# Optimization experiments

Hardware: AMD Instinct MI355X
Metric: run time of the kernel (lower is better)

## Reference

```python
import jax, jax.numpy as jnp
import numpy as np


def setup_inputs() -> dict:
    key = jax.random.key(0)
    k1, k2, k3, k4 = jax.random.split(key, 4)
    B, D, N, M = 4, 256, 4096, 4096
    return {
        "src": jax.random.normal(k1, (B, 3, N), dtype=jnp.float32),
        "tgt": jax.random.normal(k2, (B, 3, M), dtype=jnp.float32),
        "src_emb": jax.random.normal(k3, (B, D, N), dtype=jnp.float32),
        "tgt_emb": jax.random.normal(k4, (B, D, M), dtype=jnp.float32),
    }


def reference(src, tgt, src_emb, tgt_emb):
    # pairwise_distance[b,n,m] = -||src_emb[:,n] - tgt_emb[:,m]||^2
    # decomposed as -xx + 2*inner - yy (inner below is -2*dot, as in torch code)
    inner = -2.0 * jnp.einsum("bdn,bdm->bnm", src_emb, tgt_emb)       # [B,N,M]
    xx = jnp.sum(src_emb ** 2, axis=1)[:, :, None]                     # [B,N,1]
    yy = jnp.sum(tgt_emb ** 2, axis=1)[:, None, :]                     # [B,1,M]
    pairwise_distance = -xx - inner - yy                               # [B,N,M]
    scores = jax.nn.softmax(pairwise_distance, axis=2)                 # softmax over tgt points
    # src_corr[b,c,n] = sum_m tgt[b,c,m] * scores[b,n,m]
    src_corr = jnp.einsum("bcm,bnm->bcn", tgt, scores)                 # [B,3,N]
    return src_corr
```

## Files before the change

### kernel.cpp

```cpp
#include <hip/hip_runtime.h>

#define NBATCH 4
#define DDIM   256
#define NN     4096
#define MM     4096
#define NCHUNK 8
#define MCHUNK 512
#define MTILE  32
#define LOG2E  1.44269504088896340736f

using half8   = __attribute__((ext_vector_type(8))) _Float16;
using floatx4 = __attribute__((ext_vector_type(4))) float;


__global__ __launch_bounds__(256) void k_prep(const float* __restrict__ src_emb,
                                              const float* __restrict__ tgt_emb,
                                              const float* __restrict__ tgt,
                                              _Float16* __restrict__ Qf,
                                              _Float16* __restrict__ Kf,
                                              float* __restrict__ yyS,
                                              float4* __restrict__ Vt) {
    __shared__ __align__(16) float tile[128 * 64];
    __shared__ float psum[4][64];
    int i = blockIdx.x;
    int tensor = i & 1, b = (i >> 1) & 3, dg = (i >> 3) & 1, ng = i >> 4;
    int t = threadIdx.x, w = t >> 6, lane = t & 63;
    const float* in = tensor ? tgt_emb : src_emb;
    _Float16* outp  = tensor ? Kf : Qf;
    const float scale = tensor ? 1.0f : 2.0f * LOG2E;

    const char* gb = (const char*)(in + ((size_t)b * DDIM + dg * 128 + w * 32) * NN + ng * 64);
    char* lb = (char*)tile + w * 8192;
#pragma unroll
    for (int it = 0; it < 8; it++) {
        __builtin_amdgcn_global_load_lds(
            (const __attribute__((address_space(1))) uint32_t*)(const void*)
                (gb + (size_t)(it * 4 + (lane >> 4)) * (NN * 4) + (lane & 15) * 16),
            (__attribute__((address_space(3))) uint32_t*)(void*)
                (lb + it * 1024),
            16, 0, 0);
    }
    __syncthreads();

    float ss = 0.f;
    half8* ob = (half8*)(outp + (size_t)b * NN * DDIM);
    int n_glob = ng * 64 + lane;
    int blk = n_glob >> 4, l15 = n_glob & 15;
#pragma unroll
    for (int q = 0; q < 4; q++) {
        int octg = w * 4 + q;
        half8 v;
#pragma unroll
        for (int k = 0; k < 8; k++) {
            float f = tile[(octg * 8 + k) * 64 + lane];
            ss = fmaf(f, f, ss);
            v[k] = (_Float16)(f * scale);
        }
        int dglob = dg * 128 + octg * 8;
        int dsg = dglob >> 5, oct = (dglob >> 3) & 3;
        ob[(((size_t)blk * 8 + dsg) * 4 + oct) * 16 + l15] = v;
    }
    if (tensor) {
        psum[w][lane] = ss;
        __syncthreads();
        if (t < 64) {
            float s = psum[0][t] + psum[1][t] + psum[2][t] + psum[3][t];
            s *= -LOG2E;
            int m = ng * 64 + t;
            if (dg == 0) {
                const float* tp = tgt + (size_t)b * 3 * MM + m;
                Vt[(size_t)b * MM + m] = make_float4(tp[0], tp[MM], tp[2 * MM], s);
            } else {
                yyS[(size_t)b * MM + m] = s;
            }
        }
    }
}

__global__ __launch_bounds__(256, 4) void k_flash(const _Float16* __restrict__ Qf,
                                                  const _Float16* __restrict__ Kf,
                                                  const float* __restrict__ yyS,
                                                  const float4* __restrict__ Vt,
                                                  float4* __restrict__ Opart,
                                                  float* __restrict__ Mpart) {
    __shared__ __align__(16) _Float16 Kt[2][MTILE * DDIM];
    __shared__ floatx4 vtt[MCHUNK];

    int i = blockIdx.x, t = threadIdx.x;
    int xcd = i & 7, j = i >> 3;
    int b = xcd >> 1, nhalf = xcd & 1;
    int chunk = j & 7, ntile = nhalf * 16 + (j >> 3);

    int wave = t >> 6, lane = t & 63, quad = lane >> 4, l15 = lane & 15;
    int m0 = chunk * MCHUNK;
    int mblk0 = m0 >> 4;

    const char* kfb = (const char*)(Kf + (size_t)b * NN * DDIM);
    auto stage = [&](int mt) {
        const char* gb = kfb + (size_t)(mblk0 + mt * 2) * 8192 + wave * 4096;
        char* lb = (char*)&Kt[mt & 1][0] + wave * 4096;
#pragma unroll
        for (int it = 0; it < 4; it++) {
            __builtin_amdgcn_global_load_lds(
                (const __attribute__((address_space(1))) uint32_t*)(const void*)
                    (gb + it * 1024 + lane * 16),
                (__attribute__((address_space(3))) uint32_t*)(void*)
                    (lb + it * 1024),
                16, 0, 0);
        }
    };

    stage(0);

    {
        const float4* vb = Vt + (size_t)b * MM + m0;
        const float* yb = yyS + (size_t)b * MM + m0;
        for (int r = t; r < MCHUNK; r += 256) {
            float4 g = vb[r];
            vtt[r] = (floatx4){g.x, g.y, g.z, g.w + yb[r]};
        }
    }

    int nblk0 = ntile * 8 + wave * 2;
    const half8* qp = (const half8*)Qf + (size_t)b * NN * 32;
    half8 qf[2][8];
#pragma unroll
    for (int nb = 0; nb < 2; nb++)
#pragma unroll
        for (int ds = 0; ds < 8; ds++)
            qf[nb][ds] = qp[(((size_t)(nblk0 + nb) * 8 + ds) * 4 + quad) * 16 + l15];
#pragma unroll
    for (int nb = 0; nb < 2; nb++)
#pragma unroll
        for (int ds = 0; ds < 8; ds++)
            asm volatile("" : "+v"(qf[nb][ds]));

    const floatx4 z4 = {0.f, 0.f, 0.f, 0.f};
    floatx4 o[2] = {z4, z4};
    float mr[2] = {-__builtin_inff(), -__builtin_inff()};

    for (int mt = 0; mt < MCHUNK / MTILE; mt++) {
        __syncthreads();
        if (mt + 1 < MCHUNK / MTILE) stage(mt + 1);

        const char* Kb = (const char*)&Kt[mt & 1][0];
        floatx4 acc[2][2] = {{z4, z4}, {z4, z4}};
#pragma unroll
        for (int mb = 0; mb < 2; mb++) {
            const char* rb = Kb + mb * 8192 + lane * 16;
#pragma unroll
            for (int ds = 0; ds < 8; ds++) {
                half8 a = *(const half8*)(rb + ds * 1024);
                acc[mb][0] = __builtin_amdgcn_mfma_f32_16x16x32_f16(a, qf[0][ds], acc[mb][0], 0, 0, 0);
                acc[mb][1] = __builtin_amdgcn_mfma_f32_16x16x32_f16(a, qf[1][ds], acc[mb][1], 0, 0, 0);
            }
        }

        int vbase = mt * MTILE;
        float yv[8];
#pragma unroll
        for (int r = 0; r < 4; r++) {
            yv[r]     = ((const float*)&vtt[vbase + quad * 4 + r])[3];
            yv[4 + r] = ((const float*)&vtt[vbase + 16 + quad * 4 + r])[3];
        }
#pragma unroll
        for (int nb = 0; nb < 2; nb++) {
#pragma unroll
            for (int r = 0; r < 4; r++) {
                acc[0][nb][r] += yv[r];
                acc[1][nb][r] += yv[4 + r];
            }
            float tm = fmaxf(fmaxf(fmaxf(acc[0][nb][0], acc[0][nb][1]),
                                   fmaxf(acc[0][nb][2], acc[0][nb][3])),
                             fmaxf(fmaxf(acc[1][nb][0], acc[1][nb][1]),
                                   fmaxf(acc[1][nb][2], acc[1][nb][3])));
            float mn = fmaxf(mr[nb], tm);
            float al = __builtin_amdgcn_exp2f(mr[nb] - mn);
            mr[nb] = mn;
            o[nb] = o[nb] * al;
        }
#pragma unroll
        for (int jj = 0; jj < 8; jj++) {
            floatx4 vr = vtt[vbase + (jj >> 2) * 16 + quad * 4 + (jj & 3)];
#pragma unroll
            for (int nb = 0; nb < 2; nb++) {
                float p = __builtin_amdgcn_exp2f(acc[jj >> 2][nb][jj & 3] - mr[nb]);
                o[nb][0] = fmaf(p, vr[0], o[nb][0]);
                o[nb][1] = fmaf(p, vr[1], o[nb][1]);
                o[nb][2] = fmaf(p, vr[2], o[nb][2]);
                o[nb][3] += p;
            }
        }
    }

#pragma unroll
    for (int nb = 0; nb < 2; nb++) {
        float mq = mr[nb];
        float ma = fmaxf(mq, __shfl_xor(mq, 16, 64));
        ma = fmaxf(ma, __shfl_xor(ma, 32, 64));
        float wgt = __builtin_amdgcn_exp2f(mq - ma);
        floatx4 ow = o[nb] * wgt;
#pragma unroll
        for (int c = 0; c < 4; c++) {
            float v = ow[c];
            v += __shfl_xor(v, 16, 64);
            v += __shfl_xor(v, 32, 64);
            ow[c] = v;
        }
        if (quad == 0) {
            int n = (nblk0 + nb) * 16 + l15;
            size_t idx = (size_t)(chunk * NBATCH + b) * NN + n;
            Opart[idx] = make_float4(ow[0], ow[1], ow[2], ow[3]);
            Mpart[idx] = ma;
        }
    }
}

__global__ __launch_bounds__(128) void k_combine(const float4* __restrict__ Opart,
                                                 const float* __restrict__ Mpart,
                                                 float* __restrict__ out) {
    int idx = blockIdx.x * 128 + threadIdx.x;
    int b = idx >> 12, n = idx & (NN - 1);
    float mstar = -__builtin_inff();
#pragma unroll
    for (int j = 0; j < NCHUNK; j++)
        mstar = fmaxf(mstar, Mpart[(size_t)(j * NBATCH + b) * NN + n]);
    float o0 = 0.f, o1 = 0.f, o2 = 0.f, l = 0.f;
#pragma unroll
    for (int j = 0; j < NCHUNK; j++) {
        size_t id = (size_t)(j * NBATCH + b) * NN + n;
        float w = __builtin_amdgcn_exp2f(Mpart[id] - mstar);
        float4 P = Opart[id];
        o0 = fmaf(w, P.x, o0); o1 = fmaf(w, P.y, o1);
        o2 = fmaf(w, P.z, o2); l  = fmaf(w, P.w, l);
    }
    out[(size_t)(b * 3 + 0) * NN + n] = o0 / l;
    out[(size_t)(b * 3 + 1) * NN + n] = o1 / l;
    out[(size_t)(b * 3 + 2) * NN + n] = o2 / l;
}

extern "C" void kernel_launch(void* const* d_in, const int* in_sizes, int n_in,
                              void* d_out, int out_size, void* d_ws, size_t ws_size,
                              hipStream_t stream) {
    const float* tgt     = (const float*)d_in[1];
    const float* src_emb = (const float*)d_in[2];
    const float* tgt_emb = (const float*)d_in[3];
    float* out = (float*)d_out;

    char* ws = (char*)d_ws;
    _Float16* Qf  = (_Float16*)(ws);
    _Float16* Kf  = (_Float16*)(ws + 8388608);
    float*    yyS = (float*)   (ws + 16777216);
    float4*   Vt  = (float4*)  (ws + 16842752);
    float4*   Op  = (float4*)  (ws + 17104896);
    float*    Mp  = (float*)   (ws + 19202048);

    hipLaunchKernelGGL(k_prep,    dim3(1024), dim3(256), 0, stream,
                       src_emb, tgt_emb, tgt, Qf, Kf, yyS, Vt);
    hipLaunchKernelGGL(k_flash,   dim3(1024), dim3(256), 0, stream, Qf, Kf, yyS, Vt, Op, Mp);
    hipLaunchKernelGGL(k_combine, dim3(128),  dim3(128), 0, stream, Op, Mp, out);
}
```

Baseline: 133.9 us.

## Fuse Q fp16 conversion into flash kernel, drop Qf workspace pass

The prep kernel no longer converts src_emb to a blocked fp16 Qf buffer. Instead each flash block loads its query fragment straight from fp32 src_emb, scales it and converts it in registers. This removes a full write and read of the Q buffer and halves the prep grid. The cost is strided, uncoalesced fp32 loads in the flash prologue, repeated across the 8 m-chunks that share each query tile. The change also raises wave priority around the MFMA loop with s_setprio and replaces the launch-bounds occupancy hint with amdgpu_waves_per_eu(4,4).

New measurement: 152.5 us. 1.14x slower.

```diff
diff --git a/kernel.cpp b/kernel.cpp
--- a/kernel.cpp
+++ b/kernel.cpp
@@ -13,23 +13,18 @@
 using floatx4 = __attribute__((ext_vector_type(4))) float;
 
 
-__global__ __launch_bounds__(256) void k_prep(const float* __restrict__ src_emb,
-                                              const float* __restrict__ tgt_emb,
+__global__ __launch_bounds__(256) void k_prep(const float* __restrict__ tgt_emb,
                                               const float* __restrict__ tgt,
-                                              _Float16* __restrict__ Qf,
                                               _Float16* __restrict__ Kf,
                                               float* __restrict__ yyS,
                                               float4* __restrict__ Vt) {
     __shared__ __align__(16) float tile[128 * 64];
     __shared__ float psum[4][64];
     int i = blockIdx.x;
-    int tensor = i & 1, b = (i >> 1) & 3, dg = (i >> 3) & 1, ng = i >> 4;
+    int b = i & 3, dg = (i >> 2) & 1, ng = i >> 3;
     int t = threadIdx.x, w = t >> 6, lane = t & 63;
-    const float* in = tensor ? tgt_emb : src_emb;
-    _Float16* outp  = tensor ? Kf : Qf;
-    const float scale = tensor ? 1.0f : 2.0f * LOG2E;
-
-    const char* gb = (const char*)(in + ((size_t)b * DDIM + dg * 128 + w * 32) * NN + ng * 64);
+
+    const char* gb = (const char*)(tgt_emb + ((size_t)b * DDIM + dg * 128 + w * 32) * NN + ng * 64);
     char* lb = (char*)tile + w * 8192;
 #pragma unroll
     for (int it = 0; it < 8; it++) {
@@ -43,7 +38,7 @@
     __syncthreads();
 
     float ss = 0.f;
-    half8* ob = (half8*)(outp + (size_t)b * NN * DDIM);
+    half8* ob = (half8*)(Kf + (size_t)b * NN * DDIM);
     int n_glob = ng * 64 + lane;
     int blk = n_glob >> 4, l15 = n_glob & 15;
 #pragma unroll
@@ -54,35 +49,34 @@
         for (int k = 0; k < 8; k++) {
             float f = tile[(octg * 8 + k) * 64 + lane];
             ss = fmaf(f, f, ss);
-            v[k] = (_Float16)(f * scale);
+            v[k] = (_Float16)f;
         }
         int dglob = dg * 128 + octg * 8;
         int dsg = dglob >> 5, oct = (dglob >> 3) & 3;
         ob[(((size_t)blk * 8 + dsg) * 4 + oct) * 16 + l15] = v;
     }
-    if (tensor) {
-        psum[w][lane] = ss;
-        __syncthreads();
-        if (t < 64) {
-            float s = psum[0][t] + psum[1][t] + psum[2][t] + psum[3][t];
-            s *= -LOG2E;
-            int m = ng * 64 + t;
-            if (dg == 0) {
-                const float* tp = tgt + (size_t)b * 3 * MM + m;
-                Vt[(size_t)b * MM + m] = make_float4(tp[0], tp[MM], tp[2 * MM], s);
-            } else {
-                yyS[(size_t)b * MM + m] = s;
-            }
-        }
-    }
-}
-
-__global__ __launch_bounds__(256, 4) void k_flash(const _Float16* __restrict__ Qf,
-                                                  const _Float16* __restrict__ Kf,
-                                                  const float* __restrict__ yyS,
-                                                  const float4* __restrict__ Vt,
-                                                  float4* __restrict__ Opart,
-                                                  float* __restrict__ Mpart) {
+    psum[w][lane] = ss;
+    __syncthreads();
+    if (t < 64) {
+        float s = (psum[0][t] + psum[1][t]) + (psum[2][t] + psum[3][t]);
+        s *= -LOG2E;
+        int m = ng * 64 + t;
+        if (dg == 0) {
+            const float* tp = tgt + (size_t)b * 3 * MM + m;
+            Vt[(size_t)b * MM + m] = make_float4(tp[0], tp[MM], tp[2 * MM], s);
+        } else {
+            yyS[(size_t)b * MM + m] = s;
+        }
+    }
+}
+
+__global__ __launch_bounds__(256) __attribute__((amdgpu_waves_per_eu(4, 4)))
+void k_flash(const float* __restrict__ src_emb,
+             const _Float16* __restrict__ Kf,
+             const float* __restrict__ yyS,
+             const float4* __restrict__ Vt,
+             float4* __restrict__ Opart,
+             float* __restrict__ Mpart) {
     __shared__ __align__(16) _Float16 Kt[2][MTILE * DDIM];
     __shared__ floatx4 vtt[MCHUNK];
 
@@ -122,13 +116,21 @@
     }
 
     int nblk0 = ntile * 8 + wave * 2;
-    const half8* qp = (const half8*)Qf + (size_t)b * NN * 32;
+    const float* qsrc = src_emb + (size_t)b * DDIM * NN;
     half8 qf[2][8];
 #pragma unroll
-    for (int nb = 0; nb < 2; nb++)
-#pragma unroll
-        for (int ds = 0; ds < 8; ds++)
-            qf[nb][ds] = qp[(((size_t)(nblk0 + nb) * 8 + ds) * 4 + quad) * 16 + l15];
+    for (int nb = 0; nb < 2; nb++) {
+        int n = (nblk0 + nb) * 16 + l15;
+#pragma unroll
+        for (int ds = 0; ds < 8; ds++) {
+            const float* qp = qsrc + (size_t)(ds * 32 + quad * 8) * NN + n;
+            half8 v;
+#pragma unroll
+            for (int k = 0; k < 8; k++)
+                v[k] = (_Float16)(qp[(size_t)k * NN] * (2.0f * LOG2E));
+            qf[nb][ds] = v;
+        }
+    }
 #pragma unroll
     for (int nb = 0; nb < 2; nb++)
 #pragma unroll
@@ -145,6 +147,7 @@
 
         const char* Kb = (const char*)&Kt[mt & 1][0];
         floatx4 acc[2][2] = {{z4, z4}, {z4, z4}};
+        __builtin_amdgcn_s_setprio(1);
 #pragma unroll
         for (int mb = 0; mb < 2; mb++) {
             const char* rb = Kb + mb * 8192 + lane * 16;
@@ -155,6 +158,7 @@
                 acc[mb][1] = __builtin_amdgcn_mfma_f32_16x16x32_f16(a, qf[1][ds], acc[mb][1], 0, 0, 0);
             }
         }
+        __builtin_amdgcn_s_setprio(0);
 
         int vbase = mt * MTILE;
         float yv[8];
@@ -248,15 +252,15 @@
     float* out = (float*)d_out;
 
     char* ws = (char*)d_ws;
-    _Float16* Qf  = (_Float16*)(ws);
-    _Float16* Kf  = (_Float16*)(ws + 8388608);
-    float*    yyS = (float*)   (ws + 16777216);
-    float4*   Vt  = (float4*)  (ws + 16842752);
-    float4*   Op  = (float4*)  (ws + 17104896);
-    float*    Mp  = (float*)   (ws + 19202048);
-
-    hipLaunchKernelGGL(k_prep,    dim3(1024), dim3(256), 0, stream,
-                       src_emb, tgt_emb, tgt, Qf, Kf, yyS, Vt);
-    hipLaunchKernelGGL(k_flash,   dim3(1024), dim3(256), 0, stream, Qf, Kf, yyS, Vt, Op, Mp);
+    _Float16* Kf  = (_Float16*)(ws);
+    float*    yyS = (float*)   (ws + 8388608);
+    float4*   Vt  = (float4*)  (ws + 8454144);
+    float4*   Op  = (float4*)  (ws + 8716288);
+    float*    Mp  = (float*)   (ws + 10813440);
+
+    hipLaunchKernelGGL(k_prep,    dim3(512),  dim3(256), 0, stream,
+                       tgt_emb, tgt, Kf, yyS, Vt);
+    hipLaunchKernelGGL(k_flash,   dim3(1024), dim3(256), 0, stream,
+                       src_emb, Kf, yyS, Vt, Op, Mp);
     hipLaunchKernelGGL(k_combine, dim3(128),  dim3(128), 0, stream, Op, Mp, out);
 }
```

## Halve per-wave query rows in flash kernel and double grid size

Applied to the files above, without the earlier changes.

Each wave now handles one 16-row query block instead of two, so the flash kernel launches twice as many workgroups and each holds half the Q fragments and accumulators in registers. This cuts register pressure and raises parallelism, but every K tile staged into shared memory is reused by half as many MFMAs, so K traffic per output row doubles. It also raises wave priority around the MFMA loop with s_setprio and reassociates a small sum in the prep kernel.

Result: no change. 134.8 us (+0.6%).

```diff
diff --git a/kernel.cpp b/kernel.cpp
--- a/kernel.cpp
+++ b/kernel.cpp
@@ -64,7 +64,7 @@
         psum[w][lane] = ss;
         __syncthreads();
         if (t < 64) {
-            float s = psum[0][t] + psum[1][t] + psum[2][t] + psum[3][t];
+            float s = (psum[0][t] + psum[1][t]) + (psum[2][t] + psum[3][t]);
             s *= -LOG2E;
             int m = ng * 64 + t;
             if (dg == 0) {
@@ -89,7 +89,7 @@
     int i = blockIdx.x, t = threadIdx.x;
     int xcd = i & 7, j = i >> 3;
     int b = xcd >> 1, nhalf = xcd & 1;
-    int chunk = j & 7, ntile = nhalf * 16 + (j >> 3);
+    int chunk = j & 7, ntile = nhalf * 32 + (j >> 3);
 
     int wave = t >> 6, lane = t & 63, quad = lane >> 4, l15 = lane & 15;
     int m0 = chunk * MCHUNK;
@@ -121,40 +121,34 @@
         }
     }
 
-    int nblk0 = ntile * 8 + wave * 2;
+    int nblk = ntile * 4 + wave;
     const half8* qp = (const half8*)Qf + (size_t)b * NN * 32;
-    half8 qf[2][8];
-#pragma unroll
-    for (int nb = 0; nb < 2; nb++)
-#pragma unroll
-        for (int ds = 0; ds < 8; ds++)
-            qf[nb][ds] = qp[(((size_t)(nblk0 + nb) * 8 + ds) * 4 + quad) * 16 + l15];
-#pragma unroll
-    for (int nb = 0; nb < 2; nb++)
-#pragma unroll
-        for (int ds = 0; ds < 8; ds++)
-            asm volatile("" : "+v"(qf[nb][ds]));
+    half8 qf[8];
+#pragma unroll
+    for (int ds = 0; ds < 8; ds++)
+        qf[ds] = qp[(((size_t)nblk * 8 + ds) * 4 + quad) * 16 + l15];
 
     const floatx4 z4 = {0.f, 0.f, 0.f, 0.f};
-    floatx4 o[2] = {z4, z4};
-    float mr[2] = {-__builtin_inff(), -__builtin_inff()};
+    floatx4 o = z4;
+    float mr = -__builtin_inff();
 
     for (int mt = 0; mt < MCHUNK / MTILE; mt++) {
         __syncthreads();
         if (mt + 1 < MCHUNK / MTILE) stage(mt + 1);
 
         const char* Kb = (const char*)&Kt[mt & 1][0];
-        floatx4 acc[2][2] = {{z4, z4}, {z4, z4}};
+        floatx4 acc[2] = {z4, z4};
+        __builtin_amdgcn_s_setprio(1);
 #pragma unroll
         for (int mb = 0; mb < 2; mb++) {
             const char* rb = Kb + mb * 8192 + lane * 16;
 #pragma unroll
             for (int ds = 0; ds < 8; ds++) {
                 half8 a = *(const half8*)(rb + ds * 1024);
-                acc[mb][0] = __builtin_amdgcn_mfma_f32_16x16x32_f16(a, qf[0][ds], acc[mb][0], 0, 0, 0);
-                acc[mb][1] = __builtin_amdgcn_mfma_f32_16x16x32_f16(a, qf[1][ds], acc[mb][1], 0, 0, 0);
+                acc[mb] = __builtin_amdgcn_mfma_f32_16x16x32_f16(a, qf[ds], acc[mb], 0, 0, 0);
             }
         }
+        __builtin_amdgcn_s_setprio(0);
 
         int vbase = mt * MTILE;
         float yv[8];
@@ -164,42 +158,33 @@
             yv[4 + r] = ((const float*)&vtt[vbase + 16 + quad * 4 + r])[3];
         }
 #pragma unroll
-        for (int nb = 0; nb < 2; nb++) {
-#pragma unroll
-            for (int r = 0; r < 4; r++) {
-                acc[0][nb][r] += yv[r];
-                acc[1][nb][r] += yv[4 + r];
-            }
-            float tm = fmaxf(fmaxf(fmaxf(acc[0][nb][0], acc[0][nb][1]),
-                                   fmaxf(acc[0][nb][2], acc[0][nb][3])),
-                             fmaxf(fmaxf(acc[1][nb][0], acc[1][nb][1]),
-                                   fmaxf(acc[1][nb][2], acc[1][nb][3])));
-            float mn = fmaxf(mr[nb], tm);
-            float al = __builtin_amdgcn_exp2f(mr[nb] - mn);
-            mr[nb] = mn;
-            o[nb] = o[nb] * al;
-        }
+        for (int r = 0; r < 4; r++) {
+            acc[0][r] += yv[r];
+            acc[1][r] += yv[4 + r];
+        }
+        float tm = fmaxf(fmaxf(fmaxf(acc[0][0], acc[0][1]), fmaxf(acc[0][2], acc[0][3])),
+                         fmaxf(fmaxf(acc[1][0], acc[1][1]), fmaxf(acc[1][2], acc[1][3])));
+        float mn = fmaxf(mr, tm);
+        float al = __builtin_amdgcn_exp2f(mr - mn);
+        mr = mn;
+        o = o * al;
 #pragma unroll
         for (int jj = 0; jj < 8; jj++) {
             floatx4 vr = vtt[vbase + (jj >> 2) * 16 + quad * 4 + (jj & 3)];
-#pragma unroll
-            for (int nb = 0; nb < 2; nb++) {
-                float p = __builtin_amdgcn_exp2f(acc[jj >> 2][nb][jj & 3] - mr[nb]);
-                o[nb][0] = fmaf(p, vr[0], o[nb][0]);
-                o[nb][1] = fmaf(p, vr[1], o[nb][1]);
-                o[nb][2] = fmaf(p, vr[2], o[nb][2]);
-                o[nb][3] += p;
-            }
-        }
-    }
-
-#pragma unroll
-    for (int nb = 0; nb < 2; nb++) {
-        float mq = mr[nb];
+            float p = __builtin_amdgcn_exp2f(acc[jj >> 2][jj & 3] - mr);
+            o[0] = fmaf(p, vr[0], o[0]);
+            o[1] = fmaf(p, vr[1], o[1]);
+            o[2] = fmaf(p, vr[2], o[2]);
+            o[3] += p;
+        }
+    }
+
+    {
+        float mq = mr;
         float ma = fmaxf(mq, __shfl_xor(mq, 16, 64));
         ma = fmaxf(ma, __shfl_xor(ma, 32, 64));
         float wgt = __builtin_amdgcn_exp2f(mq - ma);
-        floatx4 ow = o[nb] * wgt;
+        floatx4 ow = o * wgt;
 #pragma unroll
         for (int c = 0; c < 4; c++) {
             float v = ow[c];
@@ -208,7 +193,7 @@
             ow[c] = v;
         }
         if (quad == 0) {
-            int n = (nblk0 + nb) * 16 + l15;
+            int n = nblk * 16 + l15;
             size_t idx = (size_t)(chunk * NBATCH + b) * NN + n;
             Opart[idx] = make_float4(ow[0], ow[1], ow[2], ow[3]);
             Mpart[idx] = ma;
@@ -257,6 +242,6 @@
 
     hipLaunchKernelGGL(k_prep,    dim3(1024), dim3(256), 0, stream,
                        src_emb, tgt_emb, tgt, Qf, Kf, yyS, Vt);
-    hipLaunchKernelGGL(k_flash,   dim3(1024), dim3(256), 0, stream, Qf, Kf, yyS, Vt, Op, Mp);
+    hipLaunchKernelGGL(k_flash,   dim3(2048), dim3(256), 0, stream, Qf, Kf, yyS, Vt, Op, Mp);
     hipLaunchKernelGGL(k_combine, dim3(128),  dim3(128), 0, stream, Op, Mp, out);
 }
```
